# Performance work log

Hardware: AMD Instinct MI355X
Metric: run time of the kernel (lower is better)

The kernel has to match this reference:

```python
import jax, jax.numpy as jnp
import numpy as np
from jax import lax

N_QUBITS = 8
N_LAYERS = 7


def _conv(x, w, b, stride, pad):
    y = lax.conv_general_dilated(x, w, (stride, stride), [(pad, pad), (pad, pad)],
                                 dimension_numbers=('NCHW', 'OIHW', 'NCHW'))
    return y + b[None, :, None, None]


def _apply_1q(psi, M, q):
    # psi: (B, 2,2,...,2); apply 2x2 real matrix M on qubit q (axis q+1)
    a = q + 1
    pm = jnp.moveaxis(psi, a, 1)
    out = jnp.einsum('ij,bj...->bi...', M, pm)
    return jnp.moveaxis(out, 1, a)


def _apply_cnot(psi, c, t):
    ac, at = c + 1, t + 1
    pm = jnp.moveaxis(psi, (ac, at), (1, 2))
    top = pm[:, 0]
    bot = jnp.flip(pm[:, 1], axis=1)  # flip target when control=1
    pm = jnp.stack([top, bot], axis=1)
    return jnp.moveaxis(pm, (1, 2), (ac, at))


def _quantum(features, qw):
    psi = features / jnp.linalg.norm(features, axis=1, keepdims=True)
    B = psi.shape[0]
    psi = psi.reshape((B,) + (2,) * N_QUBITS)
    for l in range(N_LAYERS):
        for q in range(N_QUBITS):
            th = qw[l, q] / 2.0
            c, s = jnp.cos(th), jnp.sin(th)
            M = jnp.stack([jnp.stack([c, -s]), jnp.stack([s, c])])
            psi = _apply_1q(psi, M, q)
        for q in range(N_QUBITS - 1):
            psi = _apply_cnot(psi, q, q + 1)
    p = psi.reshape(B, 2, -1) ** 2
    return jnp.sum(p[:, 0], axis=1) - jnp.sum(p[:, 1], axis=1)  # <PauliZ(0)>


def setup_inputs() -> dict:
    key = jax.random.key(0)
    ks = jax.random.split(key, 20)
    def g(k, shape, fan_in):
        return jax.random.normal(k, shape, jnp.float32) * (1.0 / np.sqrt(fan_in))
    inp = {
        'x':  jax.random.normal(ks[0], (4096, 1, 64, 64), jnp.float32),
        'w1': g(ks[1], (4, 1, 5, 5), 25), 'b1': jnp.zeros((4,), jnp.float32),
        'w2': g(ks[2], (8, 4, 3, 3), 36), 'b2': jnp.zeros((8,), jnp.float32),
        'w3': g(ks[3], (16, 8, 3, 3), 72), 'b3': jnp.zeros((16,), jnp.float32),
        'wf': g(ks[4], (256, 64), 64), 'bf': jnp.zeros((256,), jnp.float32),
        'qw': jax.random.uniform(ks[5], (7, 8), jnp.float32, 0.0, 2 * np.pi),
        'wc1': g(ks[6], (200, 1), 1),   'bc1': jnp.zeros((200,), jnp.float32),
        'wc2': g(ks[7], (150, 200), 200), 'bc2': jnp.zeros((150,), jnp.float32),
        'wc3': g(ks[8], (100, 150), 150), 'bc3': jnp.zeros((100,), jnp.float32),
        'wc4': g(ks[9], (50, 100), 100),  'bc4': jnp.zeros((50,), jnp.float32),
        'wc5': g(ks[10], (1, 50), 50),    'bc5': jnp.zeros((1,), jnp.float32),
    }
    return inp


def reference(x, w1, b1, w2, b2, w3, b3, wf, bf, qw,
              wc1, bc1, wc2, bc2, wc3, bc3, wc4, bc4, wc5, bc5):
    # CNN feature extractor (dropout = identity at inference)
    h = jax.nn.relu(_conv(x, w1, b1, 2, 2))   # (B,4,32,32)
    h = jax.nn.relu(_conv(h, w2, b2, 2, 1))   # (B,8,16,16)
    h = jax.nn.relu(_conv(h, w3, b3, 1, 1))   # (B,16,16,16)
    B = h.shape[0]
    # AdaptiveAvgPool2d(2): 16x16 -> 2x2 via 8x8 non-overlapping means
    h = h.reshape(B, 16, 2, 8, 2, 8).mean(axis=(3, 5))  # (B,16,2,2)
    h = h.reshape(B, 64)
    feats = jax.nn.relu(h @ wf.T + bf)        # (B,256)
    # F.normalize(p=2, dim=1)
    feats = feats / jnp.maximum(jnp.linalg.norm(feats, axis=1, keepdims=True), 1e-12)
    # Batched 8-qubit statevector simulation (replaces per-sample Python loop)
    q = _quantum(feats, qw)[:, None]          # (B,1)
    # MLP classifier
    h = jax.nn.relu(q @ wc1.T + bc1)
    h = jax.nn.relu(h @ wc2.T + bc2)
    h = jax.nn.relu(h @ wc3.T + bc3)
    h = jax.nn.relu(h @ wc4.T + bc4)
    return jax.nn.sigmoid(h @ wc5.T + bc5)    # (B,1)
```

## Files before the change

kernel.cpp:

```cpp
#include <hip/hip_runtime.h>
#include <math.h>

typedef float v2f __attribute__((ext_vector_type(2)));
#define FMA2(a, b, c) __builtin_elementwise_fma((a), (b), (c))

__global__ __launch_bounds__(256, 6)
void convpool_kernel(const float* __restrict__ x,
                     const float* __restrict__ w1, const float* __restrict__ b1,
                     const float* __restrict__ w2, const float* __restrict__ b2,
                     const float* __restrict__ w3, const float* __restrict__ b3,
                     float* __restrict__ poolout)
{
    __shared__ __align__(16) float arena[4620];
    __shared__ __align__(16) float w3s[1168];
    const int tid  = threadIdx.x;
    const int b    = blockIdx.x;
    const int lane = tid & 63;

    for (int i = tid; i < 1168; i += 256) w3s[i] = (i < 1152) ? w3[i] : b3[i - 1152];
    for (int i = tid; i < 140; i += 256) { int oc = i / 35, c = i - oc * 35; arena[oc * 1155 + c] = 0.f; }
    for (int i = tid; i < 132; i += 256) { int oc = i / 33, r = i - oc * 33; arena[oc * 1155 + r * 35] = 0.f; }

    {
        const float* xb = x + (size_t)b * 4096;
        const int oh  = tid >> 3;
        const int ow  = tid & 7;
        const int ow0 = ow * 4;
        const int c0  = ow0 * 2 - 2;
        const bool cmL = (ow == 0);
        const bool cmR = (ow == 7);
        v2f a01[4], a23[4];
        #pragma unroll
        for (int oc = 0; oc < 4; oc++) {
            const float bv = b1[oc];
            a01[oc] = (v2f){bv, bv};
            a23[oc] = (v2f){bv, bv};
        }
        #pragma unroll
        for (int kh = 0; kh < 5; kh++) {
            const int ih = oh * 2 - 2 + kh;
            if (ih >= 0 && ih < 64) {
                const float* row = xb + ih * 64;
                float colv[11];
                {
                    float v0 = row[cmL ? 0 : c0];
                    float v1 = row[cmL ? 0 : c0 + 1];
                    float vA = row[cmR ? 63 : c0 + 10];
                    colv[0]  = cmL ? 0.f : v0;
                    colv[1]  = cmL ? 0.f : v1;
                    colv[10] = cmR ? 0.f : vA;
                }
                #pragma unroll
                for (int cc = 2; cc < 10; cc++) colv[cc] = row[c0 + cc];
                #pragma unroll
                for (int kw = 0; kw < 5; kw++) {
                    const v2f c01 = {colv[kw],     colv[kw + 2]};
                    const v2f c23 = {colv[kw + 4], colv[kw + 6]};
                    #pragma unroll
                    for (int oc = 0; oc < 4; oc++) {
                        const float wv = w1[oc * 25 + kh * 5 + kw];
                        const v2f ws = {wv, wv};
                        a01[oc] = FMA2(c01, ws, a01[oc]);
                        a23[oc] = FMA2(c23, ws, a23[oc]);
                    }
                }
            }
        }
        #pragma unroll
        for (int oc = 0; oc < 4; oc++) {
            float* o = arena + oc * 1155 + (oh + 1) * 35 + ow0 + 1;
            o[0] = fmaxf(a01[oc].x, 0.f); o[1] = fmaxf(a01[oc].y, 0.f);
            o[2] = fmaxf(a23[oc].x, 0.f); o[3] = fmaxf(a23[oc].y, 0.f);
        }
    }
    __syncthreads();

    v2f rA01, rA23, rB01, rB23;
    {
        const int oc0 = __builtin_amdgcn_readfirstlane(tid >> 6);
        const int oh  = lane >> 2, ow0 = (lane & 3) * 4;
        {
            const float ba = b2[oc0], bb = b2[oc0 + 4];
            rA01 = (v2f){ba, ba}; rA23 = (v2f){ba, ba};
            rB01 = (v2f){bb, bb}; rB23 = (v2f){bb, bb};
        }
        const int c0s = ow0 * 2;
        #pragma unroll
        for (int ic = 0; ic < 4; ic++) {
            const float* base = arena + ic * 1155;
            #pragma unroll
            for (int kh = 0; kh < 3; kh++) {
                const int ihs = oh * 2 + kh;
                float colv[9];
                #pragma unroll
                for (int cc = 0; cc < 9; cc++) colv[cc] = base[ihs * 35 + c0s + cc];
                #pragma unroll
                for (int kw = 0; kw < 3; kw++) {
                    const v2f c01 = {colv[kw],     colv[kw + 2]};
                    const v2f c23 = {colv[kw + 4], colv[kw + 6]};
                    const float wa = w2[((oc0    ) * 4 + ic) * 9 + kh * 3 + kw];
                    const float wb = w2[((oc0 + 4) * 4 + ic) * 9 + kh * 3 + kw];
                    const v2f was = {wa, wa}, wbs = {wb, wb};
                    rA01 = FMA2(c01, was, rA01);
                    rA23 = FMA2(c23, was, rA23);
                    rB01 = FMA2(c01, wbs, rB01);
                    rB23 = FMA2(c23, wbs, rB23);
                }
            }
        }
    }
    __syncthreads();

    for (int i = tid; i < 576; i += 256) {
        const int ch = i / 72, j = i - ch * 72;
        if (j < 18)      arena[ch * 324 + j] = 0.f;
        else if (j < 36) arena[ch * 324 + 17 * 18 + (j - 18)] = 0.f;
        else if (j < 52) arena[ch * 324 + (j - 35) * 18] = 0.f;
        else if (j < 68) arena[ch * 324 + (j - 51) * 18 + 17] = 0.f;
    }
    {
        const int oc0 = __builtin_amdgcn_readfirstlane(tid >> 6);
        const int oh  = lane >> 2, ow0 = (lane & 3) * 4;
        float* oA = arena + oc0 * 324       + (oh + 1) * 18 + ow0 + 1;
        float* oB = arena + (oc0 + 4) * 324 + (oh + 1) * 18 + ow0 + 1;
        oA[0] = fmaxf(rA01.x, 0.f); oA[1] = fmaxf(rA01.y, 0.f);
        oA[2] = fmaxf(rA23.x, 0.f); oA[3] = fmaxf(rA23.y, 0.f);
        oB[0] = fmaxf(rB01.x, 0.f); oB[1] = fmaxf(rB01.y, 0.f);
        oB[2] = fmaxf(rB23.x, 0.f); oB[3] = fmaxf(rB23.y, 0.f);
    }
    __syncthreads();

    {
        const int oc = tid >> 4, s = tid & 15;
        const int tr = (s >> 2) * 4, tc = (s & 3) * 4;
        v2f acc2[4][2];
        const float bv = w3s[1152 + oc];
        #pragma unroll
        for (int r = 0; r < 4; r++) {
            acc2[r][0] = (v2f){bv, bv};
            acc2[r][1] = (v2f){bv, bv};
        }
        #pragma unroll
        for (int ic = 0; ic < 8; ic++) {
            const float* xc = arena + ic * 324;
            float p[6][6];
            #pragma unroll
            for (int dr = 0; dr < 6; dr++)
                #pragma unroll
                for (int dc = 0; dc < 6; dc++)
                    p[dr][dc] = xc[(tr + dr) * 18 + (tc + dc)];
            float wv[9];
            #pragma unroll
            for (int k = 0; k < 9; k++) wv[k] = w3s[oc * 72 + ic * 9 + k];
            #pragma unroll
            for (int r = 0; r < 4; r++) {
                #pragma unroll
                for (int c2 = 0; c2 < 2; c2++) {
                    const int cb = c2 * 2;
                    v2f a = acc2[r][c2];
                    #pragma unroll
                    for (int kh = 0; kh < 3; kh++) {
                        const int rr = r + kh;
                        #pragma unroll
                        for (int kw = 0; kw < 3; kw++) {
                            const v2f pp = {p[rr][cb + kw], p[rr][cb + kw + 1]};
                            const float w = wv[kh * 3 + kw];
                            const v2f ws = {w, w};
                            a = FMA2(pp, ws, a);
                        }
                    }
                    acc2[r][c2] = a;
                }
            }
        }
        float ps = 0.f;
        #pragma unroll
        for (int r = 0; r < 4; r++) {
            ps += fmaxf(acc2[r][0].x, 0.f);
            ps += fmaxf(acc2[r][0].y, 0.f);
            ps += fmaxf(acc2[r][1].x, 0.f);
            ps += fmaxf(acc2[r][1].y, 0.f);
        }
        ps += __shfl_xor(ps, 1, 64);
        ps += __shfl_xor(ps, 4, 64);
        if ((s & 5) == 0) {
            const int ii = s >> 3, jj = (s >> 1) & 1;
            poolout[b * 64 + oc * 4 + ii * 2 + jj] = ps * (1.f / 64.f);
        }
    }
}

__global__ __launch_bounds__(256)
void head_kernel(const float* __restrict__ poolin,
                 const float* __restrict__ wf, const float* __restrict__ bf,
                 const float* __restrict__ qw,
                 const float* __restrict__ wc1, const float* __restrict__ bc1,
                 const float* __restrict__ wc2, const float* __restrict__ bc2,
                 const float* __restrict__ wc3, const float* __restrict__ bc3,
                 const float* __restrict__ wc4, const float* __restrict__ bc4,
                 const float* __restrict__ wc5, const float* __restrict__ bc5,
                 float* __restrict__ out)
{
    __shared__ __align__(16) float pool_s[256];
    __shared__ __align__(16) float feats[1024];
    __shared__ __align__(16) float h1[800];
    __shared__ __align__(16) float h2[600];
    __shared__ __align__(16) float h3[400];
    __shared__ __align__(16) float h4[200];
    __shared__ float zbuf[4];
    __shared__ float csc[56], css[56];

    const int tid  = threadIdx.x;
    const int blk  = blockIdx.x;
    const int lane = tid & 63;
    const int wv   = tid >> 6;

    pool_s[tid] = poolin[(size_t)blk * 256 + tid];
    if (tid < 56) {
        float th = qw[tid] * 0.5f;
        csc[tid] = cosf(th);
        css[tid] = sinf(th);
    }
    __syncthreads();

    {
        float acc[4];
        const float bv = bf[tid];
        #pragma unroll
        for (int e = 0; e < 4; e++) acc[e] = bv;
        const float4* wr = (const float4*)(wf + tid * 64);
        #pragma unroll
        for (int kc = 0; kc < 4; kc++) {
            float4 w0 = wr[kc * 4 + 0], w1_ = wr[kc * 4 + 1], w2_ = wr[kc * 4 + 2], w3_ = wr[kc * 4 + 3];
            #pragma unroll
            for (int e = 0; e < 4; e++) {
                const float4* pp = (const float4*)(pool_s + e * 64 + kc * 16);
                float4 p0 = pp[0], p1 = pp[1], p2 = pp[2], p3 = pp[3];
                float a = acc[e];
                a = fmaf(w0.x, p0.x, a); a = fmaf(w0.y, p0.y, a); a = fmaf(w0.z, p0.z, a); a = fmaf(w0.w, p0.w, a);
                a = fmaf(w1_.x, p1.x, a); a = fmaf(w1_.y, p1.y, a); a = fmaf(w1_.z, p1.z, a); a = fmaf(w1_.w, p1.w, a);
                a = fmaf(w2_.x, p2.x, a); a = fmaf(w2_.y, p2.y, a); a = fmaf(w2_.z, p2.z, a); a = fmaf(w2_.w, p2.w, a);
                a = fmaf(w3_.x, p3.x, a); a = fmaf(w3_.y, p3.y, a); a = fmaf(w3_.z, p3.z, a); a = fmaf(w3_.w, p3.w, a);
                acc[e] = a;
            }
        }
        #pragma unroll
        for (int e = 0; e < 4; e++) feats[e * 256 + tid] = fmaxf(acc[e], 0.f);
    }
    __syncthreads();

    {
        const float* base = feats + wv * 256;
        float v0 = base[lane], v1 = base[64 + lane];
        float v2 = base[128 + lane], v3 = base[192 + lane];
        float ssq = v0 * v0 + v1 * v1 + v2 * v2 + v3 * v3;
        #pragma unroll
        for (int off = 1; off < 64; off <<= 1) ssq += __shfl_xor(ssq, off, 64);
        const float inv = 1.0f / fmaxf(sqrtf(ssq), 1e-12f);
        v0 *= inv; v1 *= inv; v2 *= inv; v3 *= inv;

        for (int l = 0; l < 7; l++) {
            {
                float c = csc[l * 8 + 0], s = css[l * 8 + 0];
                float n0 = c * v0 - s * v2, n2 = s * v0 + c * v2;
                float n1 = c * v1 - s * v3, n3 = s * v1 + c * v3;
                float c1 = csc[l * 8 + 1], s1 = css[l * 8 + 1];
                v0 = c1 * n0 - s1 * n1; v1 = s1 * n0 + c1 * n1;
                v2 = c1 * n2 - s1 * n3; v3 = s1 * n2 + c1 * n3;
            }
            #pragma unroll
            for (int q = 2; q < 8; q++) {
                const int m = 1 << (7 - q);
                const float c = csc[l * 8 + q], s = css[l * 8 + q];
                const float sgn = (lane & m) ? s : -s;
                float t0 = __shfl_xor(v0, m, 64);
                float t1 = __shfl_xor(v1, m, 64);
                float t2 = __shfl_xor(v2, m, 64);
                float t3 = __shfl_xor(v3, m, 64);
                v0 = fmaf(sgn, t0, c * v0);
                v1 = fmaf(sgn, t1, c * v1);
                v2 = fmaf(sgn, t2, c * v2);
                v3 = fmaf(sgn, t3, c * v3);
            }
            { float t = v2; v2 = v3; v3 = t; }
            v1 = __shfl_xor(v1, 32, 64);
            v3 = __shfl_xor(v3, 32, 64);
            #pragma unroll
            for (int q = 2; q < 7; q++) {
                const int mc = 1 << (7 - q), mt = 1 << (6 - q);
                float t0 = __shfl_xor(v0, mt, 64);
                float t1 = __shfl_xor(v1, mt, 64);
                float t2 = __shfl_xor(v2, mt, 64);
                float t3 = __shfl_xor(v3, mt, 64);
                if (lane & mc) { v0 = t0; v1 = t1; v2 = t2; v3 = t3; }
            }
        }
        float m0 = v0 * v0 + v1 * v1 - v2 * v2 - v3 * v3;
        #pragma unroll
        for (int off = 1; off < 64; off <<= 1) m0 += __shfl_xor(m0, off, 64);
        if (lane == 0) zbuf[wv] = m0;
    }
    __syncthreads();

    if (tid < 200) {
        const float w = wc1[tid], bv = bc1[tid];
        #pragma unroll
        for (int e = 0; e < 4; e++) h1[e * 200 + tid] = fmaxf(fmaf(zbuf[e], w, bv), 0.f);
    }
    __syncthreads();
    if (tid < 150) {
        float acc[4];
        const float bv = bc2[tid];
        #pragma unroll
        for (int e = 0; e < 4; e++) acc[e] = bv;
        const float4* wr = (const float4*)(wc2 + tid * 200);
        for (int kc = 0; kc < 25; kc++) {
            float4 wa = wr[2 * kc], wb = wr[2 * kc + 1];
            #pragma unroll
            for (int e = 0; e < 4; e++) {
                const float4* hp = (const float4*)(h1 + e * 200) + 2 * kc;
                float4 ha = hp[0], hb = hp[1];
                float a = acc[e];
                a = fmaf(wa.x, ha.x, a); a = fmaf(wa.y, ha.y, a); a = fmaf(wa.z, ha.z, a); a = fmaf(wa.w, ha.w, a);
                a = fmaf(wb.x, hb.x, a); a = fmaf(wb.y, hb.y, a); a = fmaf(wb.z, hb.z, a); a = fmaf(wb.w, hb.w, a);
                acc[e] = a;
            }
        }
        #pragma unroll
        for (int e = 0; e < 4; e++) h2[e * 150 + tid] = fmaxf(acc[e], 0.f);
    }
    __syncthreads();
    if (tid < 100) {
        float acc[4];
        const float bv = bc3[tid];
        #pragma unroll
        for (int e = 0; e < 4; e++) acc[e] = bv;
        const float2* wr = (const float2*)(wc3 + tid * 150);
        for (int k = 0; k < 75; k++) {
            float2 wa = wr[k];
            #pragma unroll
            for (int e = 0; e < 4; e++) {
                float2 hv = ((const float2*)(h2 + e * 150))[k];
                acc[e] = fmaf(wa.x, hv.x, fmaf(wa.y, hv.y, acc[e]));
            }
        }
        #pragma unroll
        for (int e = 0; e < 4; e++) h3[e * 100 + tid] = fmaxf(acc[e], 0.f);
    }
    __syncthreads();
    if (tid < 50) {
        float acc[4];
        const float bv = bc4[tid];
        #pragma unroll
        for (int e = 0; e < 4; e++) acc[e] = bv;
        const float4* wr = (const float4*)(wc4 + tid * 100);
        for (int kc = 0; kc < 25; kc++) {
            float4 wa = wr[kc];
            #pragma unroll
            for (int e = 0; e < 4; e++) {
                float4 hv = ((const float4*)(h3 + e * 100))[kc];
                float a = acc[e];
                a = fmaf(wa.x, hv.x, a); a = fmaf(wa.y, hv.y, a);
                a = fmaf(wa.z, hv.z, a); a = fmaf(wa.w, hv.w, a);
                acc[e] = a;
            }
        }
        #pragma unroll
        for (int e = 0; e < 4; e++) h4[e * 50 + tid] = fmaxf(acc[e], 0.f);
    }
    __syncthreads();
    if (tid < 4) {
        float acc = bc5[0];
        const float2* wr = (const float2*)wc5;
        #pragma unroll
        for (int k = 0; k < 25; k++) {
            float2 wa = wr[k];
            float2 hv = ((const float2*)(h4 + tid * 50))[k];
            acc = fmaf(wa.x, hv.x, fmaf(wa.y, hv.y, acc));
        }
        out[blk * 4 + tid] = 1.0f / (1.0f + expf(-acc));
    }
}

extern "C" void kernel_launch(void* const* d_in, const int* in_sizes, int n_in,
                              void* d_out, int out_size, void* d_ws, size_t ws_size,
                              hipStream_t stream) {
    const float* x   = (const float*)d_in[0];
    const float* w1  = (const float*)d_in[1];
    const float* b1  = (const float*)d_in[2];
    const float* w2  = (const float*)d_in[3];
    const float* b2  = (const float*)d_in[4];
    const float* w3  = (const float*)d_in[5];
    const float* b3  = (const float*)d_in[6];
    const float* wf  = (const float*)d_in[7];
    const float* bf  = (const float*)d_in[8];
    const float* qw  = (const float*)d_in[9];
    const float* wc1 = (const float*)d_in[10];
    const float* bc1 = (const float*)d_in[11];
    const float* wc2 = (const float*)d_in[12];
    const float* bc2 = (const float*)d_in[13];
    const float* wc3 = (const float*)d_in[14];
    const float* bc3 = (const float*)d_in[15];
    const float* wc4 = (const float*)d_in[16];
    const float* bc4 = (const float*)d_in[17];
    const float* wc5 = (const float*)d_in[18];
    const float* bc5 = (const float*)d_in[19];
    float* out = (float*)d_out;

    float* poolbuf = (float*)d_ws;

    convpool_kernel<<<4096, 256, 0, stream>>>(x, w1, b1, w2, b2, w3, b3, poolbuf);
    head_kernel<<<1024, 256, 0, stream>>>(poolbuf, wf, bf, qw,
                                          wc1, bc1, wc2, bc2, wc3, bc3,
                                          wc4, bc4, wc5, bc5, out);
}
```

Baseline: 217.3 us.

## Give conv2/conv3 threads more output channels each, use half the threads

```diff
diff --git a/kernel.cpp b/kernel.cpp
--- a/kernel.cpp
+++ b/kernel.cpp
@@ -12,12 +12,17 @@
                      float* __restrict__ poolout)
 {
     __shared__ __align__(16) float arena[4620];
-    __shared__ __align__(16) float w3s[1168];
+    __shared__ __align__(16) float w3p[1552];
     const int tid  = threadIdx.x;
     const int b    = blockIdx.x;
     const int lane = tid & 63;
 
-    for (int i = tid; i < 1168; i += 256) w3s[i] = (i < 1152) ? w3[i] : b3[i - 1152];
+    for (int i = tid; i < 1152; i += 256) {
+        int oc = i / 72, r = i - oc * 72;
+        int ic = r / 9,  k = r - ic * 9;
+        w3p[oc * 96 + ic * 12 + k] = w3[i];
+    }
+    if (tid < 16) w3p[1536 + tid] = b3[tid];
     for (int i = tid; i < 140; i += 256) { int oc = i / 35, c = i - oc * 35; arena[oc * 1155 + c] = 0.f; }
     for (int i = tid; i < 132; i += 256) { int oc = i / 33, r = i - oc * 33; arena[oc * 1155 + r * 35] = 0.f; }
 
@@ -75,36 +80,39 @@
     }
     __syncthreads();
 
-    v2f rA01, rA23, rB01, rB23;
+    v2f c2acc[4][2];
     {
-        const int oc0 = __builtin_amdgcn_readfirstlane(tid >> 6);
-        const int oh  = lane >> 2, ow0 = (lane & 3) * 4;
-        {
-            const float ba = b2[oc0], bb = b2[oc0 + 4];
-            rA01 = (v2f){ba, ba}; rA23 = (v2f){ba, ba};
-            rB01 = (v2f){bb, bb}; rB23 = (v2f){bb, bb};
-        }
-        const int c0s = ow0 * 2;
-        #pragma unroll
-        for (int ic = 0; ic < 4; ic++) {
-            const float* base = arena + ic * 1155;
-            #pragma unroll
-            for (int kh = 0; kh < 3; kh++) {
-                const int ihs = oh * 2 + kh;
-                float colv[9];
+        if (tid < 128) {
+            const int ocg = __builtin_amdgcn_readfirstlane(tid >> 6);
+            const int oh  = lane >> 2, ow0 = (lane & 3) * 4;
+            #pragma unroll
+            for (int i = 0; i < 4; i++) {
+                const float bv = b2[ocg * 4 + i];
+                c2acc[i][0] = (v2f){bv, bv};
+                c2acc[i][1] = (v2f){bv, bv};
+            }
+            const int c0s = ow0 * 2;
+            #pragma unroll
+            for (int ic = 0; ic < 4; ic++) {
+                const float* base = arena + ic * 1155;
                 #pragma unroll
-                for (int cc = 0; cc < 9; cc++) colv[cc] = base[ihs * 35 + c0s + cc];
-                #pragma unroll
-                for (int kw = 0; kw < 3; kw++) {
-                    const v2f c01 = {colv[kw],     colv[kw + 2]};
-                    const v2f c23 = {colv[kw + 4], colv[kw + 6]};
-                    const float wa = w2[((oc0    ) * 4 + ic) * 9 + kh * 3 + kw];
-                    const float wb = w2[((oc0 + 4) * 4 + ic) * 9 + kh * 3 + kw];
-                    const v2f was = {wa, wa}, wbs = {wb, wb};
-                    rA01 = FMA2(c01, was, rA01);
-                    rA23 = FMA2(c23, was, rA23);
-                    rB01 = FMA2(c01, wbs, rB01);
-                    rB23 = FMA2(c23, wbs, rB23);
+                for (int kh = 0; kh < 3; kh++) {
+                    const int ihs = oh * 2 + kh;
+                    float colv[9];
+                    #pragma unroll
+                    for (int cc = 0; cc < 9; cc++) colv[cc] = base[ihs * 35 + c0s + cc];
+                    #pragma unroll
+                    for (int kw = 0; kw < 3; kw++) {
+                        const v2f c01 = {colv[kw],     colv[kw + 2]};
+                        const v2f c23 = {colv[kw + 4], colv[kw + 6]};
+                        #pragma unroll
+                        for (int i = 0; i < 4; i++) {
+                            const float wv = w2[((ocg * 4 + i) * 4 + ic) * 9 + kh * 3 + kw];
+                            const v2f ws = {wv, wv};
+                            c2acc[i][0] = FMA2(c01, ws, c2acc[i][0]);
+                            c2acc[i][1] = FMA2(c23, ws, c2acc[i][1]);
+                        }
+                    }
                 }
             }
         }
@@ -118,74 +126,84 @@
         else if (j < 52) arena[ch * 324 + (j - 35) * 18] = 0.f;
         else if (j < 68) arena[ch * 324 + (j - 51) * 18 + 17] = 0.f;
     }
-    {
-        const int oc0 = __builtin_amdgcn_readfirstlane(tid >> 6);
+    if (tid < 128) {
+        const int ocg = tid >> 6;
         const int oh  = lane >> 2, ow0 = (lane & 3) * 4;
-        float* oA = arena + oc0 * 324       + (oh + 1) * 18 + ow0 + 1;
-        float* oB = arena + (oc0 + 4) * 324 + (oh + 1) * 18 + ow0 + 1;
-        oA[0] = fmaxf(rA01.x, 0.f); oA[1] = fmaxf(rA01.y, 0.f);
-        oA[2] = fmaxf(rA23.x, 0.f); oA[3] = fmaxf(rA23.y, 0.f);
-        oB[0] = fmaxf(rB01.x, 0.f); oB[1] = fmaxf(rB01.y, 0.f);
-        oB[2] = fmaxf(rB23.x, 0.f); oB[3] = fmaxf(rB23.y, 0.f);
-    }
-    __syncthreads();
-
-    {
-        const int oc = tid >> 4, s = tid & 15;
+        #pragma unroll
+        for (int i = 0; i < 4; i++) {
+            float* o = arena + (ocg * 4 + i) * 324 + (oh + 1) * 18 + ow0 + 1;
+            o[0] = fmaxf(c2acc[i][0].x, 0.f); o[1] = fmaxf(c2acc[i][0].y, 0.f);
+            o[2] = fmaxf(c2acc[i][1].x, 0.f); o[3] = fmaxf(c2acc[i][1].y, 0.f);
+        }
+    }
+    __syncthreads();
+
+    if (tid < 128) {
+        const int op = tid >> 4;
+        const int s  = tid & 15;
         const int tr = (s >> 2) * 4, tc = (s & 3) * 4;
-        v2f acc2[4][2];
-        const float bv = w3s[1152 + oc];
-        #pragma unroll
-        for (int r = 0; r < 4; r++) {
-            acc2[r][0] = (v2f){bv, bv};
-            acc2[r][1] = (v2f){bv, bv};
+        const int ocA = op * 2, ocB = ocA + 1;
+        v2f accA[4][2], accB[4][2];
+        {
+            const float bvA = w3p[1536 + ocA], bvB = w3p[1536 + ocB];
+            #pragma unroll
+            for (int r = 0; r < 4; r++) {
+                accA[r][0] = (v2f){bvA, bvA}; accA[r][1] = (v2f){bvA, bvA};
+                accB[r][0] = (v2f){bvB, bvB}; accB[r][1] = (v2f){bvB, bvB};
+            }
         }
         #pragma unroll
         for (int ic = 0; ic < 8; ic++) {
             const float* xc = arena + ic * 324;
-            float p[6][6];
-            #pragma unroll
-            for (int dr = 0; dr < 6; dr++)
+            const float4 wA0 = *(const float4*)(w3p + ocA * 96 + ic * 12);
+            const float4 wA1 = *(const float4*)(w3p + ocA * 96 + ic * 12 + 4);
+            const float  wA8 = w3p[ocA * 96 + ic * 12 + 8];
+            const float4 wB0 = *(const float4*)(w3p + ocB * 96 + ic * 12);
+            const float4 wB1 = *(const float4*)(w3p + ocB * 96 + ic * 12 + 4);
+            const float  wB8 = w3p[ocB * 96 + ic * 12 + 8];
+            const float wA[9] = {wA0.x, wA0.y, wA0.z, wA0.w, wA1.x, wA1.y, wA1.z, wA1.w, wA8};
+            const float wB[9] = {wB0.x, wB0.y, wB0.z, wB0.w, wB1.x, wB1.y, wB1.z, wB1.w, wB8};
+            #pragma unroll
+            for (int dr = 0; dr < 6; dr++) {
+                const float2* rp = (const float2*)(xc + (tr + dr) * 18 + tc);
+                const float2 q0 = rp[0], q1 = rp[1], q2 = rp[2];
+                const float prow[6] = {q0.x, q0.y, q1.x, q1.y, q2.x, q2.y};
                 #pragma unroll
-                for (int dc = 0; dc < 6; dc++)
-                    p[dr][dc] = xc[(tr + dr) * 18 + (tc + dc)];
-            float wv[9];
-            #pragma unroll
-            for (int k = 0; k < 9; k++) wv[k] = w3s[oc * 72 + ic * 9 + k];
-            #pragma unroll
-            for (int r = 0; r < 4; r++) {
-                #pragma unroll
-                for (int c2 = 0; c2 < 2; c2++) {
-                    const int cb = c2 * 2;
-                    v2f a = acc2[r][c2];
-                    #pragma unroll
-                    for (int kh = 0; kh < 3; kh++) {
-                        const int rr = r + kh;
+                for (int kh = 0; kh < 3; kh++) {
+                    const int r = dr - kh;
+                    if (r >= 0 && r < 4) {
                         #pragma unroll
-                        for (int kw = 0; kw < 3; kw++) {
-                            const v2f pp = {p[rr][cb + kw], p[rr][cb + kw + 1]};
-                            const float w = wv[kh * 3 + kw];
-                            const v2f ws = {w, w};
-                            a = FMA2(pp, ws, a);
+                        for (int c2 = 0; c2 < 2; c2++) {
+                            const int cb = c2 * 2;
+                            v2f aA = accA[r][c2], aB = accB[r][c2];
+                            #pragma unroll
+                            for (int kw = 0; kw < 3; kw++) {
+                                const v2f pp  = {prow[cb + kw], prow[cb + kw + 1]};
+                                const v2f wAs = {wA[kh * 3 + kw], wA[kh * 3 + kw]};
+                                const v2f wBs = {wB[kh * 3 + kw], wB[kh * 3 + kw]};
+                                aA = FMA2(pp, wAs, aA);
+                                aB = FMA2(pp, wBs, aB);
+                            }
+                            accA[r][c2] = aA; accB[r][c2] = aB;
                         }
                     }
-                    acc2[r][c2] = a;
                 }
             }
         }
-        float ps = 0.f;
+        float psA = 0.f, psB = 0.f;
         #pragma unroll
         for (int r = 0; r < 4; r++) {
-            ps += fmaxf(acc2[r][0].x, 0.f);
-            ps += fmaxf(acc2[r][0].y, 0.f);
-            ps += fmaxf(acc2[r][1].x, 0.f);
-            ps += fmaxf(acc2[r][1].y, 0.f);
-        }
-        ps += __shfl_xor(ps, 1, 64);
-        ps += __shfl_xor(ps, 4, 64);
+            psA += fmaxf(accA[r][0].x, 0.f); psA += fmaxf(accA[r][0].y, 0.f);
+            psA += fmaxf(accA[r][1].x, 0.f); psA += fmaxf(accA[r][1].y, 0.f);
+            psB += fmaxf(accB[r][0].x, 0.f); psB += fmaxf(accB[r][0].y, 0.f);
+            psB += fmaxf(accB[r][1].x, 0.f); psB += fmaxf(accB[r][1].y, 0.f);
+        }
+        psA += __shfl_xor(psA, 1, 64); psA += __shfl_xor(psA, 4, 64);
+        psB += __shfl_xor(psB, 1, 64); psB += __shfl_xor(psB, 4, 64);
         if ((s & 5) == 0) {
             const int ii = s >> 3, jj = (s >> 1) & 1;
-            poolout[b * 64 + oc * 4 + ii * 2 + jj] = ps * (1.f / 64.f);
+            poolout[b * 64 + ocA * 4 + ii * 2 + jj] = psA * (1.f / 64.f);
+            poolout[b * 64 + ocB * 4 + ii * 2 + jj] = psB * (1.f / 64.f);
         }
     }
 }
```

Result: slower. 224.0 us (+3.1%).
